# Optimization experiments

Measured on AMD Instinct MI355X. Metric: run time of the kernel, lower is better.

The kernel has to match this reference:

```python
import jax, jax.numpy as jnp
import numpy as np

NUM_HEADS = 16


def setup_inputs() -> dict:
    key = jax.random.key(0)
    ks = jax.random.split(key, 7)
    B, S, H = 4, 2048, 1024
    scale = 1.0 / np.sqrt(H)
    return {
        "hidden_states": jax.random.normal(ks[0], (B, S, H), dtype=jnp.float32),
        "attention_mask": jnp.ones((B, S), dtype=jnp.int32),
        "Wq": jax.random.normal(ks[1], (H, H), dtype=jnp.float32) * scale,
        "bq": jnp.zeros((H,), dtype=jnp.float32),
        "Wk": jax.random.normal(ks[2], (H, H), dtype=jnp.float32) * scale,
        "bk": jnp.zeros((H,), dtype=jnp.float32),
        "Wv": jax.random.normal(ks[3], (H, H), dtype=jnp.float32) * scale,
        "bv": jnp.zeros((H,), dtype=jnp.float32),
    }


def _split_heads(x, n_heads):
    B, S, H = x.shape
    return x.reshape(B, S, n_heads, H // n_heads).transpose(0, 2, 1, 3)  # [B,h,S,d]


def reference(hidden_states, attention_mask, Wq, bq, Wk, bk, Wv, bv):
    B, S, H = hidden_states.shape
    dh = H // NUM_HEADS
    # nn.Linear applies x @ W.T + b
    q = _split_heads(hidden_states @ Wq.T + bq, NUM_HEADS)
    k = _split_heads(hidden_states @ Wk.T + bk, NUM_HEADS)
    v = _split_heads(hidden_states @ Wv.T + bv, NUM_HEADS)
    scores = jnp.einsum("bhqd,bhkd->bhqk", q, k)  # [B,h,S,S]
    # masked_fill with -inf before scaling == masking after scaling
    mask = attention_mask[:, None, None, :] == 0
    scores = jnp.where(mask, -jnp.inf, scores)
    probs = jax.nn.softmax(scores / jnp.sqrt(jnp.float32(dh)), axis=-1)
    out = jnp.einsum("bhqk,bhkd->bhqd", probs, v)  # [B,h,S,d]
    return out.transpose(0, 2, 1, 3).reshape(B, S, H)
```

## Files before the change

### kernel.cpp

```cpp
#include <hip/hip_runtime.h>
#include <hip/hip_bf16.h>
#include <stdint.h>

constexpr int CB  = 4;
constexpr int CS  = 2048;
constexpr int CH  = 1024;
constexpr int CNH = 16;
constexpr int CDH = 64;
constexpr int CM  = CB * CS;

typedef __bf16 bf16x8 __attribute__((ext_vector_type(8)));
typedef float  f32x4  __attribute__((ext_vector_type(4)));

__device__ __forceinline__ unsigned short f2bf(float f) {
    union { float f; unsigned u; } c; c.f = f;
    unsigned u = c.u;
    unsigned r = (u + 0x7fffu + ((u >> 16) & 1u)) >> 16;
    return (unsigned short)r;
}

__device__ __forceinline__ void gl_lds16(const void* g, void* l) {
    __builtin_amdgcn_global_load_lds((const __attribute__((address_space(1))) uint32_t*)g,
                                     (__attribute__((address_space(3))) uint32_t*)l,
                                     16, 0, 0);
}

__device__ __forceinline__ float fexp2(float x) {
#if __has_builtin(__builtin_amdgcn_exp2f)
    return __builtin_amdgcn_exp2f(x);
#else
    return exp2f(x);
#endif
}

__device__ __forceinline__ unsigned vperm(unsigned s0, unsigned s1, unsigned sel) {
#if __has_builtin(__builtin_amdgcn_perm)
    return __builtin_amdgcn_perm(s0, s1, sel);
#else
    unsigned r = 0;
    for (int k = 0; k < 4; k++) {
        unsigned idx = (sel >> (8 * k)) & 0xff;
        unsigned byte = (idx < 4) ? (s1 >> (8 * idx)) : (s0 >> (8 * (idx - 4)));
        r |= (byte & 0xff) << (8 * k);
    }
    return r;
#endif
}
__device__ __forceinline__ unsigned pack_hihalf(unsigned lo_u, unsigned hi_u) {
    return vperm(hi_u, lo_u, 0x07060302u);
}

constexpr float C_SC = 0.125f * 1.44269504f;

__global__ __launch_bounds__(256) void cvt_all(const float* __restrict__ hs,
                                               const float* __restrict__ w0,
                                               const float* __restrict__ w1,
                                               const float* __restrict__ w2,
                                               unsigned short* __restrict__ Xb,
                                               unsigned short* __restrict__ Wb) {
    int z = blockIdx.y;
    const float* src; unsigned short* dst; int n4;
    if (z == 0)      { src = hs; dst = Xb;              n4 = CM * CH / 4; }
    else if (z == 1) { src = w0; dst = Wb;              n4 = CH * CH / 4; }
    else if (z == 2) { src = w1; dst = Wb + CH * CH;    n4 = CH * CH / 4; }
    else             { src = w2; dst = Wb + 2 * CH * CH; n4 = CH * CH / 4; }
    int i = blockIdx.x * blockDim.x + threadIdx.x;
    if (i < n4) {
        float4 v = ((const float4*)src)[i];
        ushort4 o;
        o.x = f2bf(v.x); o.y = f2bf(v.y); o.z = f2bf(v.z); o.w = f2bf(v.w);
        ((ushort4*)dst)[i] = o;
    }
}

__global__ __launch_bounds__(256) void qkv_gemm(
    const unsigned short* __restrict__ Xb,
    const unsigned short* __restrict__ Wb,
    const float* __restrict__ bq, const float* __restrict__ bk, const float* __restrict__ bv,
    unsigned short* __restrict__ Qo,
    unsigned short* __restrict__ Ko,
    unsigned short* __restrict__ Vt)
{
    __shared__ alignas(16) unsigned char smem[34816];
    typedef unsigned short (*tile_t)[128][32];
    tile_t As = (tile_t)smem;
    tile_t Bs = (tile_t)(smem + 16384);
    typedef unsigned short (*ep_t)[136];
    ep_t Ep = (ep_t)smem;

    const int tid  = threadIdx.x;
    const int wave = tid >> 6, lane = tid & 63;
    const int wm = wave >> 1, wn = wave & 1;
    const int col = lane & 15, quad = lane >> 4;
    const int gm = blockIdx.x * 128, gn = blockIdx.y * 128;
    const int z  = blockIdx.z;
    const unsigned short* W = Wb + (size_t)z * CH * CH;

    f32x4 zero = {0.f, 0.f, 0.f, 0.f};
    f32x4 acc[4][4];
    for (int i = 0; i < 4; i++) for (int j = 0; j < 4; j++) acc[i][j] = zero;

    const int arow = lane >> 2;
    const int acol = (lane & 3) * 8;

    auto stage = [&](int buf, int k0) {
        for (int c = 0; c < 2; ++c) {
            int r0 = wave * 32 + c * 16;
            gl_lds16(Xb + (size_t)(gm + r0 + arow) * CH + k0 + acol, &As[buf][r0][0]);
            gl_lds16(W  + (size_t)(gn + r0 + arow) * CH + k0 + acol, &Bs[buf][r0][0]);
        }
    };

    stage(0, 0);
    for (int kk = 0; kk < 32; ++kk) {
        int cur = kk & 1;
        __syncthreads();
        if (kk < 31) stage(cur ^ 1, (kk + 1) * 32);
        bf16x8 af[4], bfm[4];
        for (int i = 0; i < 4; i++)
            af[i] = *(const bf16x8*)&As[cur][wm * 64 + i * 16 + col][quad * 8];
        for (int j = 0; j < 4; j++)
            bfm[j] = *(const bf16x8*)&Bs[cur][wn * 64 + j * 16 + col][quad * 8];
        for (int i = 0; i < 4; i++)
            for (int j = 0; j < 4; j++)
                acc[i][j] = __builtin_amdgcn_mfma_f32_16x16x32_bf16(af[i], bfm[j], acc[i][j], 0, 0, 0);
    }

    __syncthreads();

    const float* bias = (z == 0) ? bq : (z == 1) ? bk : bv;
    const int bb = gm >> 11, ss0 = gm & 2047;
    const int h0 = gn >> 6;

    if (z == 2) {
        for (int j = 0; j < 4; j++) {
            int nl = wn * 64 + j * 16 + col;
            float bias_v = bias[gn + nl];
            for (int i = 0; i < 4; i++) {
                int ml = wm * 64 + i * 16 + quad * 4;
                unsigned d0 = (unsigned)f2bf(acc[i][j][0] + bias_v) |
                              ((unsigned)f2bf(acc[i][j][1] + bias_v) << 16);
                unsigned d1 = (unsigned)f2bf(acc[i][j][2] + bias_v) |
                              ((unsigned)f2bf(acc[i][j][3] + bias_v) << 16);
                *(unsigned*)&Ep[nl][ml]     = d0;
                *(unsigned*)&Ep[nl][ml + 2] = d1;
            }
        }
        __syncthreads();
        for (int p = 0; p < 8; p++) {
            int nl = p * 16 + (tid >> 4);
            int seg = tid & 15;
            uint4 v = *(const uint4*)&Ep[nl][seg * 8];
            int h = h0 + (nl >> 6), d = nl & 63;
            *(uint4*)(Vt + ((size_t)(bb * CNH + h) * CDH + d) * CS + ss0 + seg * 8) = v;
        }
    } else {
        const float mulf = (z == 0) ? C_SC : 1.0f;
        for (int j = 0; j < 4; j++) {
            int nl = wn * 64 + j * 16 + col;
            float bias_v = bias[gn + nl];
            for (int i = 0; i < 4; i++)
                for (int r = 0; r < 4; r++) {
                    int ml = wm * 64 + i * 16 + quad * 4 + r;
                    Ep[ml][nl] = f2bf((acc[i][j][r] + bias_v) * mulf);
                }
        }
        __syncthreads();
        unsigned short* dst01 = (z == 0) ? Qo : Ko;
        for (int p = 0; p < 8; p++) {
            int ml = p * 16 + (tid >> 4);
            int half = (tid >> 3) & 1, seg = tid & 7;
            uint4 v = *(const uint4*)&Ep[ml][half * 64 + seg * 8];
            int h = h0 + half;
            *(uint4*)(dst01 + ((size_t)(bb * CNH + h) * CS + ss0 + ml) * CDH + seg * 8) = v;
        }
    }
}

__global__ __launch_bounds__(256, 2) void flash_attn(
    const unsigned short* __restrict__ Q,
    const unsigned short* __restrict__ K,
    const unsigned short* __restrict__ Vt,
    const int* __restrict__ mask,
    float* __restrict__ out)
{
    __shared__ alignas(16) unsigned short Ks[2][64][64];
    __shared__ alignas(16) unsigned short Vs[2][64][64];
    __shared__ alignas(16) unsigned int   Ps[4][64][32];
    __shared__ unsigned int Mbits[64];

    const int tid  = threadIdx.x;
    const int wave = tid >> 6, lane = tid & 63;
    const int col = lane & 15, quad = lane >> 4;
    const int bh = blockIdx.y;
    const int bI = bh >> 4, hI = bh & 15;
    const int q0 = blockIdx.x * 256 + wave * 64;

    const unsigned short* Qp = Q  + (size_t)bh * CS * CDH;
    const unsigned short* Kp = K  + (size_t)bh * CS * CDH;
    const unsigned short* Vp = Vt + (size_t)bh * CDH * CS;

    {
        const int* mg = mask + bI * CS;
        for (int j = 0; j < 8; j++) {
            int idx = wave * 512 + j * 64 + lane;
            unsigned long long bal = __ballot(mg[idx] != 0);
            if (lane == 0) {
                Mbits[wave * 16 + j * 2]     = (unsigned int)bal;
                Mbits[wave * 16 + j * 2 + 1] = (unsigned int)(bal >> 32);
            }
        }
    }

    bf16x8 aq[4][2];
    for (int i = 0; i < 4; i++)
        for (int ks = 0; ks < 2; ks++)
            aq[i][ks] = *(const bf16x8*)(Qp + (size_t)(q0 + i * 16 + col) * CDH + ks * 32 + quad * 8);

    bf16x8 onesb;
    {
        union { unsigned short u; __bf16 b; } ob; ob.u = 0x3F80;
        for (int j = 0; j < 8; j++) onesb[j] = ob.b;
    }

    f32x4 zero = {0.f, 0.f, 0.f, 0.f};
    f32x4 o[4][4], lfr[4];
    for (int i = 0; i < 4; i++) {
        lfr[i] = zero;
        for (int id = 0; id < 4; id++) o[i][id] = zero;
    }

    const int srow = lane >> 3;
    const int schk = (lane & 7) ^ srow;

    auto stageKV = [&](int buf, int t) {
        const unsigned short* kg = Kp + (size_t)t * 64 * CDH;
        for (int c = 0; c < 2; c++) {
            int r0 = wave * 16 + c * 8;
            gl_lds16(kg + (size_t)(r0 + srow) * CDH + schk * 8, &Ks[buf][r0][0]);
            gl_lds16(Vp + (size_t)(r0 + srow) * CS + t * 64 + schk * 8, &Vs[buf][r0][0]);
        }
    };

    stageKV(0, 0);
    for (int kt = 0; kt < 32; ++kt) {
        int cur = kt & 1;
        __syncthreads();
        if (kt < 31) stageKV(cur ^ 1, kt + 1);

        f32x4 sfr[4][4];
        for (int i = 0; i < 4; i++) for (int ik = 0; ik < 4; ik++) sfr[i][ik] = zero;
        for (int ks = 0; ks < 2; ks++) {
            bf16x8 bkf[4];
            for (int ik = 0; ik < 4; ik++)
                bkf[ik] = *(const bf16x8*)&Ks[cur][ik * 16 + col][((ks * 4 + quad) ^ (col & 7)) * 8];
            for (int i = 0; i < 4; i++)
                for (int ik = 0; ik < 4; ik++)
                    sfr[i][ik] = __builtin_amdgcn_mfma_f32_16x16x32_bf16(aq[i][ks], bkf[ik], sfr[i][ik], 0, 0, 0);
        }

        unsigned int w0 = Mbits[kt * 2], w1 = Mbits[kt * 2 + 1];
        if ((w0 & w1) != 0xFFFFFFFFu) {
            float madd[4];
            madd[0] = ((w0 >> col) & 1u)        ? 0.f : -1.0e30f;
            madd[1] = ((w0 >> (col + 16)) & 1u) ? 0.f : -1.0e30f;
            madd[2] = ((w1 >> col) & 1u)        ? 0.f : -1.0e30f;
            madd[3] = ((w1 >> (col + 16)) & 1u) ? 0.f : -1.0e30f;
            for (int i = 0; i < 4; i++)
                for (int ik = 0; ik < 4; ik++)
                    for (int r = 0; r < 4; r++)
                        sfr[i][ik][r] += madd[ik];
        }

        for (int i = 0; i < 4; i++)
            for (int ik = 0; ik < 2; ik++)
                for (int r = 0; r < 4; r++) {
                    union { float f; unsigned u; } a, b;
                    a.f = fexp2(sfr[i][ik][r]);
                    b.f = fexp2(sfr[i][ik + 2][r]);
                    unsigned dw = pack_hihalf(a.u, b.u);
                    int row = i * 16 + quad * 4 + r;
                    int p = ik * 16 + col;
                    Ps[wave][row][(((p >> 2) ^ (row & 7)) << 2) + (p & 3)] = dw;
                }

        for (int i = 0; i < 4; i++) {
            const unsigned* base = &Ps[wave][i * 16 + col][0];
            uint4 w0v = *(const uint4*)(base + (((quad * 2 + 0) ^ (col & 7)) << 2));
            uint4 w1v = *(const uint4*)(base + (((quad * 2 + 1) ^ (col & 7)) << 2));
            uint4 lo, hi;
            lo.x = vperm(w0v.y, w0v.x, 0x05040100u); hi.x = vperm(w0v.y, w0v.x, 0x07060302u);
            lo.y = vperm(w0v.w, w0v.z, 0x05040100u); hi.y = vperm(w0v.w, w0v.z, 0x07060302u);
            lo.z = vperm(w1v.y, w1v.x, 0x05040100u); hi.z = vperm(w1v.y, w1v.x, 0x07060302u);
            lo.w = vperm(w1v.w, w1v.z, 0x05040100u); hi.w = vperm(w1v.w, w1v.z, 0x07060302u);
            bf16x8 ap0, ap1;
            __builtin_memcpy(&ap0, &lo, 16);
            __builtin_memcpy(&ap1, &hi, 16);

            for (int ks = 0; ks < 2; ks++) {
                bf16x8 ap = (ks == 0) ? ap0 : ap1;
                bf16x8 bvf[4];
                for (int id = 0; id < 4; id++)
                    bvf[id] = *(const bf16x8*)&Vs[cur][id * 16 + col][((ks * 4 + quad) ^ (col & 7)) * 8];
                for (int id = 0; id < 4; id++)
                    o[i][id] = __builtin_amdgcn_mfma_f32_16x16x32_bf16(ap, bvf[id], o[i][id], 0, 0, 0);
                lfr[i] = __builtin_amdgcn_mfma_f32_16x16x32_bf16(ap, onesb, lfr[i], 0, 0, 0);
            }
        }
    }

    for (int i = 0; i < 4; i++)
        for (int r = 0; r < 4; r++) {
            int sI = q0 + i * 16 + quad * 4 + r;
            float inv = 1.0f / lfr[i][r];
            for (int id = 0; id < 4; id++)
                out[((size_t)(bI * CS + sI)) * CH + hI * CDH + id * 16 + col] = o[i][id][r] * inv;
        }
}

extern "C" void kernel_launch(void* const* d_in, const int* in_sizes, int n_in,
                              void* d_out, int out_size, void* d_ws, size_t ws_size,
                              hipStream_t stream) {
    const float* hs  = (const float*)d_in[0];
    const int*  mask = (const int*)d_in[1];
    const float* Wq  = (const float*)d_in[2];
    const float* bq  = (const float*)d_in[3];
    const float* Wk  = (const float*)d_in[4];
    const float* bk  = (const float*)d_in[5];
    const float* Wv  = (const float*)d_in[6];
    const float* bv  = (const float*)d_in[7];
    float* out = (float*)d_out;

    char* ws = (char*)d_ws;
    unsigned short* Xb = (unsigned short*)(ws);
    unsigned short* Wb = (unsigned short*)(ws + 16777216);
    unsigned short* Qb = (unsigned short*)(ws + 23068672);
    unsigned short* Kb = (unsigned short*)(ws + 39845888);
    unsigned short* Vt = (unsigned short*)(ws + 56623104);

    cvt_all<<<dim3(8192, 4), 256, 0, stream>>>(hs, Wq, Wk, Wv, Xb, Wb);

    qkv_gemm<<<dim3(CM / 128, CH / 128, 3), 256, 0, stream>>>(Xb, Wb, bq, bk, bv, Qb, Kb, Vt);

    flash_attn<<<dim3(CS / 256, CB * CNH), 256, 0, stream>>>(Qb, Kb, Vt, mask, out);
}
```

Measured before the change: 261.6 us.

## Swizzle QKV GEMM LDS tiles, halve epilogue buffer, hoist V fragment loads

```diff
diff --git a/kernel.cpp b/kernel.cpp
--- a/kernel.cpp
+++ b/kernel.cpp
@@ -73,7 +73,7 @@
     }
 }
 
-__global__ __launch_bounds__(256) void qkv_gemm(
+__global__ __launch_bounds__(256, 4) void qkv_gemm(
     const unsigned short* __restrict__ Xb,
     const unsigned short* __restrict__ Wb,
     const float* __restrict__ bq, const float* __restrict__ bk, const float* __restrict__ bv,
@@ -81,7 +81,7 @@
     unsigned short* __restrict__ Ko,
     unsigned short* __restrict__ Vt)
 {
-    __shared__ alignas(16) unsigned char smem[34816];
+    __shared__ alignas(16) unsigned char smem[32768];
     typedef unsigned short (*tile_t)[128][32];
     tile_t As = (tile_t)smem;
     tile_t Bs = (tile_t)(smem + 16384);
@@ -100,16 +100,18 @@
     f32x4 acc[4][4];
     for (int i = 0; i < 4; i++) for (int j = 0; j < 4; j++) acc[i][j] = zero;
 
-    const int arow = lane >> 2;
-    const int acol = (lane & 3) * 8;
+    const int arow  = lane >> 2;
+    const int schnk = (lane & 3) ^ (arow & 3);
 
     auto stage = [&](int buf, int k0) {
         for (int c = 0; c < 2; ++c) {
             int r0 = wave * 32 + c * 16;
-            gl_lds16(Xb + (size_t)(gm + r0 + arow) * CH + k0 + acol, &As[buf][r0][0]);
-            gl_lds16(W  + (size_t)(gn + r0 + arow) * CH + k0 + acol, &Bs[buf][r0][0]);
+            gl_lds16(Xb + (size_t)(gm + r0 + arow) * CH + k0 + schnk * 8, &As[buf][r0][0]);
+            gl_lds16(W  + (size_t)(gn + r0 + arow) * CH + k0 + schnk * 8, &Bs[buf][r0][0]);
         }
     };
+
+    const int rchnk = quad ^ (col & 3);
 
     stage(0, 0);
     for (int kk = 0; kk < 32; ++kk) {
@@ -118,61 +120,70 @@
         if (kk < 31) stage(cur ^ 1, (kk + 1) * 32);
         bf16x8 af[4], bfm[4];
         for (int i = 0; i < 4; i++)
-            af[i] = *(const bf16x8*)&As[cur][wm * 64 + i * 16 + col][quad * 8];
+            af[i] = *(const bf16x8*)&As[cur][wm * 64 + i * 16 + col][rchnk * 8];
         for (int j = 0; j < 4; j++)
-            bfm[j] = *(const bf16x8*)&Bs[cur][wn * 64 + j * 16 + col][quad * 8];
+            bfm[j] = *(const bf16x8*)&Bs[cur][wn * 64 + j * 16 + col][rchnk * 8];
         for (int i = 0; i < 4; i++)
             for (int j = 0; j < 4; j++)
                 acc[i][j] = __builtin_amdgcn_mfma_f32_16x16x32_bf16(af[i], bfm[j], acc[i][j], 0, 0, 0);
     }
 
-    __syncthreads();
-
     const float* bias = (z == 0) ? bq : (z == 1) ? bk : bv;
     const int bb = gm >> 11, ss0 = gm & 2047;
     const int h0 = gn >> 6;
 
     if (z == 2) {
-        for (int j = 0; j < 4; j++) {
-            int nl = wn * 64 + j * 16 + col;
-            float bias_v = bias[gn + nl];
-            for (int i = 0; i < 4; i++) {
-                int ml = wm * 64 + i * 16 + quad * 4;
-                unsigned d0 = (unsigned)f2bf(acc[i][j][0] + bias_v) |
-                              ((unsigned)f2bf(acc[i][j][1] + bias_v) << 16);
-                unsigned d1 = (unsigned)f2bf(acc[i][j][2] + bias_v) |
-                              ((unsigned)f2bf(acc[i][j][3] + bias_v) << 16);
-                *(unsigned*)&Ep[nl][ml]     = d0;
-                *(unsigned*)&Ep[nl][ml + 2] = d1;
-            }
-        }
-        __syncthreads();
-        for (int p = 0; p < 8; p++) {
-            int nl = p * 16 + (tid >> 4);
-            int seg = tid & 15;
-            uint4 v = *(const uint4*)&Ep[nl][seg * 8];
-            int h = h0 + (nl >> 6), d = nl & 63;
-            *(uint4*)(Vt + ((size_t)(bb * CNH + h) * CDH + d) * CS + ss0 + seg * 8) = v;
+        for (int hn = 0; hn < 2; hn++) {
+            __syncthreads();
+            if (wn == hn) {
+                for (int j = 0; j < 4; j++) {
+                    int nl = j * 16 + col;
+                    float bias_v = bias[gn + hn * 64 + nl];
+                    for (int i = 0; i < 4; i++) {
+                        int ml = wm * 64 + i * 16 + quad * 4;
+                        unsigned d0 = (unsigned)f2bf(acc[i][j][0] + bias_v) |
+                                      ((unsigned)f2bf(acc[i][j][1] + bias_v) << 16);
+                        unsigned d1 = (unsigned)f2bf(acc[i][j][2] + bias_v) |
+                                      ((unsigned)f2bf(acc[i][j][3] + bias_v) << 16);
+                        *(unsigned*)&Ep[nl][ml]     = d0;
+                        *(unsigned*)&Ep[nl][ml + 2] = d1;
+                    }
+                }
+            }
+            __syncthreads();
+            for (int p = 0; p < 4; p++) {
+                int nl = p * 16 + (tid >> 4);
+                int seg = tid & 15;
+                uint4 v = *(const uint4*)&Ep[nl][seg * 8];
+                int h = h0 + hn, d = nl;
+                *(uint4*)(Vt + ((size_t)(bb * CNH + h) * CDH + d) * CS + ss0 + seg * 8) = v;
+            }
         }
     } else {
         const float mulf = (z == 0) ? C_SC : 1.0f;
-        for (int j = 0; j < 4; j++) {
-            int nl = wn * 64 + j * 16 + col;
-            float bias_v = bias[gn + nl];
-            for (int i = 0; i < 4; i++)
-                for (int r = 0; r < 4; r++) {
-                    int ml = wm * 64 + i * 16 + quad * 4 + r;
-                    Ep[ml][nl] = f2bf((acc[i][j][r] + bias_v) * mulf);
+        unsigned short* dst01 = (z == 0) ? Qo : Ko;
+        for (int hm = 0; hm < 2; hm++) {
+            __syncthreads();
+            if (wm == hm) {
+                for (int j = 0; j < 4; j++) {
+                    int nl = wn * 64 + j * 16 + col;
+                    float bias_v = bias[gn + nl];
+                    for (int i = 0; i < 4; i++)
+                        for (int r = 0; r < 4; r++) {
+                            int ml = i * 16 + quad * 4 + r;
+                            Ep[ml][nl] = f2bf((acc[i][j][r] + bias_v) * mulf);
+                        }
                 }
-        }
-        __syncthreads();
-        unsigned short* dst01 = (z == 0) ? Qo : Ko;
-        for (int p = 0; p < 8; p++) {
-            int ml = p * 16 + (tid >> 4);
-            int half = (tid >> 3) & 1, seg = tid & 7;
-            uint4 v = *(const uint4*)&Ep[ml][half * 64 + seg * 8];
-            int h = h0 + half;
-            *(uint4*)(dst01 + ((size_t)(bb * CNH + h) * CS + ss0 + ml) * CDH + seg * 8) = v;
+            }
+            __syncthreads();
+            for (int p = 0; p < 4; p++) {
+                int mlRel = p * 16 + (tid >> 4);
+                int ml = hm * 64 + mlRel;
+                int half = (tid >> 3) & 1, seg = tid & 7;
+                uint4 v = *(const uint4*)&Ep[mlRel][half * 64 + seg * 8];
+                int h = h0 + half;
+                *(uint4*)(dst01 + ((size_t)(bb * CNH + h) * CS + ss0 + ml) * CDH + seg * 8) = v;
+            }
         }
     }
 }
@@ -283,6 +294,11 @@
                     int p = ik * 16 + col;
                     Ps[wave][row][(((p >> 2) ^ (row & 7)) << 2) + (p & 3)] = dw;
                 }
+
+        bf16x8 bvf2[2][4];
+        for (int ks = 0; ks < 2; ks++)
+            for (int id = 0; id < 4; id++)
+                bvf2[ks][id] = *(const bf16x8*)&Vs[cur][id * 16 + col][((ks * 4 + quad) ^ (col & 7)) * 8];
 
         for (int i = 0; i < 4; i++) {
             const unsigned* base = &Ps[wave][i * 16 + col][0];
@@ -299,11 +315,8 @@
 
             for (int ks = 0; ks < 2; ks++) {
                 bf16x8 ap = (ks == 0) ? ap0 : ap1;
-                bf16x8 bvf[4];
                 for (int id = 0; id < 4; id++)
-                    bvf[id] = *(const bf16x8*)&Vs[cur][id * 16 + col][((ks * 4 + quad) ^ (col & 7)) * 8];
-                for (int id = 0; id < 4; id++)
-                    o[i][id] = __builtin_amdgcn_mfma_f32_16x16x32_bf16(ap, bvf[id], o[i][id], 0, 0, 0);
+                    o[i][id] = __builtin_amdgcn_mfma_f32_16x16x32_bf16(ap, bvf2[ks][id], o[i][id], 0, 0, 0);
                 lfr[i] = __builtin_amdgcn_mfma_f32_16x16x32_bf16(ap, onesb, lfr[i], 0, 0, 0);
             }
         }
```

Measured after the change: 262.7 us. About the same (+0.4%).
